# Kernel optimization log

Measured on AMD Instinct MI355X. Metric: run time of the kernel, lower is better.

Reference implementation:

```python
import jax, jax.numpy as jnp
import numpy as np
from jax import lax

EPS = 1e-5

def quantize_ternary(w):
    # scale = mean(|w|).clamp_min(1e-5) computed on detached weight
    scale = jnp.maximum(jnp.mean(jnp.abs(lax.stop_gradient(w))), EPS)
    ws = w / scale
    # STE: forward uses round+clamp, backward is identity in ws
    wq = lax.stop_gradient(jnp.clip(jnp.round(ws), -1.0, 1.0) - ws) + ws
    return wq * scale

def conv2d(x, w, b):
    # x: [N,C,H,W], w: [O,I,kh,kw], stride 1, pad 1 -> same spatial size
    out = lax.conv_general_dilated(
        x, w, window_strides=(1, 1), padding=[(1, 1), (1, 1)],
        dimension_numbers=("NCHW", "OIHW", "NCHW"))
    return out + b[None, :, None, None]

def setup_inputs() -> dict:
    key = jax.random.key(0)
    k1, k2, k3, k4, k5 = jax.random.split(key, 5)
    N, C_in, C_out, H, W, K = 16, 64, 64, 128, 128, 3
    fan_in = C_in * K * K
    bound = 1.0 / np.sqrt(fan_in)
    x = jax.random.normal(k1, (N, C_in, H, W), dtype=jnp.float32)
    w = jax.random.uniform(k2, (C_out, C_in, K, K), minval=-bound, maxval=bound, dtype=jnp.float32)
    b = jax.random.uniform(k3, (C_out,), minval=-bound, maxval=bound, dtype=jnp.float32)
    # growth child: kaiming-uniform-like init scaled by 0.01, zero bias
    w_child = jax.random.uniform(k4, (C_out, C_in, K, K), minval=-bound, maxval=bound, dtype=jnp.float32) * 0.01
    b_child = jnp.zeros((C_out,), dtype=jnp.float32)
    gate = jnp.zeros((1,), dtype=jnp.float32)  # growth_gate buffer
    return {"x": x, "w": w, "b": b, "w_child": w_child, "b_child": b_child, "gate": gate}

def reference(x, w, b, w_child, b_child, gate):
    out = conv2d(x, quantize_ternary(w), b)
    child_out = conv2d(x, quantize_ternary(w_child), b_child)
    g = jax.nn.sigmoid(gate)  # shape [1], broadcasts
    return out + g * child_out
```

## Files before the change

kernel.cpp:

```cpp
#include <hip/hip_runtime.h>
#include <math.h>


typedef __attribute__((ext_vector_type(8))) short short8;
typedef __attribute__((ext_vector_type(4))) float float4v;

__device__ inline unsigned short f2bf(float f) {
  union { float f; unsigned u; } v; v.f = f;
  unsigned u = v.u;
  return (unsigned short)((u + 0x7FFFu + ((u >> 16) & 1u)) >> 16);
}

__global__ __launch_bounds__(256) void prep(
    const float* __restrict__ w, const float* __restrict__ wc,
    const float* __restrict__ b, const float* __restrict__ bc,
    const float* __restrict__ gate,
    unsigned short* __restrict__ wq, float* __restrict__ beff) {
  const int tid = threadIdx.x;
  const float4v* w4 = (const float4v*)w;
  const float4v* c4 = (const float4v*)wc;
  double a0 = 0, a1 = 0, a2 = 0, a3 = 0;
  double c0 = 0, c1 = 0, c2 = 0, c3 = 0;
#pragma unroll
  for (int i = 0; i < 36; i += 4) {
    float4v wa = w4[tid + (i + 0) * 256];
    float4v wb = w4[tid + (i + 1) * 256];
    float4v wcv = w4[tid + (i + 2) * 256];
    float4v wd = w4[tid + (i + 3) * 256];
    float4v xa = c4[tid + (i + 0) * 256];
    float4v xb = c4[tid + (i + 1) * 256];
    float4v xc = c4[tid + (i + 2) * 256];
    float4v xd = c4[tid + (i + 3) * 256];
    a0 += (double)fabsf(wa[0]) + (double)fabsf(wa[1]) + (double)fabsf(wa[2]) + (double)fabsf(wa[3]);
    a1 += (double)fabsf(wb[0]) + (double)fabsf(wb[1]) + (double)fabsf(wb[2]) + (double)fabsf(wb[3]);
    a2 += (double)fabsf(wcv[0]) + (double)fabsf(wcv[1]) + (double)fabsf(wcv[2]) + (double)fabsf(wcv[3]);
    a3 += (double)fabsf(wd[0]) + (double)fabsf(wd[1]) + (double)fabsf(wd[2]) + (double)fabsf(wd[3]);
    c0 += (double)fabsf(xa[0]) + (double)fabsf(xa[1]) + (double)fabsf(xa[2]) + (double)fabsf(xa[3]);
    c1 += (double)fabsf(xb[0]) + (double)fabsf(xb[1]) + (double)fabsf(xb[2]) + (double)fabsf(xb[3]);
    c2 += (double)fabsf(xc[0]) + (double)fabsf(xc[1]) + (double)fabsf(xc[2]) + (double)fabsf(xc[3]);
    c3 += (double)fabsf(xd[0]) + (double)fabsf(xd[1]) + (double)fabsf(xd[2]) + (double)fabsf(xd[3]);
  }
  double a = (a0 + a1) + (a2 + a3);
  double c = (c0 + c1) + (c2 + c3);
#pragma unroll
  for (int off = 32; off > 0; off >>= 1) {
    a += __shfl_down(a, off);
    c += __shfl_down(c, off);
  }
  __shared__ double sa[4], sc[4];
  const int wv = tid >> 6;
  if ((tid & 63) == 0) { sa[wv] = a; sc[wv] = c; }
  __syncthreads();
  const double ta = (sa[0] + sa[1]) + (sa[2] + sa[3]);
  const double tc = (sc[0] + sc[1]) + (sc[2] + sc[3]);
  const float sw = fmaxf((float)(ta * (1.0 / 36864.0)), 1e-5f);
  const float scl = fmaxf((float)(tc * (1.0 / 36864.0)), 1e-5f);
  const float g = 1.0f / (1.0f + expf(-gate[0]));
  const int idx = blockIdx.x * 256 + tid;
  const int tap = idx >> 12;
  const int oc = (idx >> 6) & 63;
  const int ci = idx & 63;
  const int src = oc * 576 + ci * 9 + tap;
  float q1 = fminf(1.f, fmaxf(-1.f, rintf(w[src] / sw))) * sw;
  float q2 = fminf(1.f, fmaxf(-1.f, rintf(wc[src] / scl))) * scl;
  wq[idx] = f2bf(q1 + g * q2);
  if (idx < 64) beff[idx] = b[idx] + g * bc[idx];
}

__global__ __launch_bounds__(512, 4) void conv_fused(
    const float* __restrict__ x, const unsigned short* __restrict__ wq,
    const float* __restrict__ beff, float* __restrict__ out) {
  extern __shared__ __align__(16) char smem[];
  char* Abase = smem;
  char* Bbase = smem + 65536;

  const int bid = blockIdx.x;
  const int xcd = bid & 7;
  const int u = bid >> 3;
  const int n = xcd * 2 + (u >> 6);
  const int h0 = (u & 63) * 2;
  const int tid = threadIdx.x;
  const int lane = tid & 63;
  const int wv = tid >> 6;
  const int rw = wv >> 2;
  const int pxh = ((wv >> 1) & 1) * 64;
  const int och = (wv & 1) * 32;
  const int ln15 = lane & 15;
  const int lq = lane >> 4;

  const float* xn = x + (size_t)n * (64 * 16384);

  const short8 b0v = *(const short8*)(wq + tid * 8);

  const int pxc = tid & 127;
  const int hi = tid >> 7;
#pragma unroll
  for (int grp = 0; grp < 2; ++grp) {
    float t[4][8];
#pragma unroll
    for (int j = 0; j < 4; ++j) {
      const int k = grp * 16 + j * 4 + hi;
      const int r = k >> 3;
      const int c = k & 7;
      const int h = h0 + r - 1;
      if ((unsigned)h < 128u) {
        const float* sp = xn + c * 8 * 16384 + h * 128 + pxc;
#pragma unroll
        for (int e = 0; e < 8; ++e) t[j][e] = sp[e * 16384];
      } else {
#pragma unroll
        for (int e = 0; e < 8; ++e) t[j][e] = 0.f;
      }
    }
#pragma unroll
    for (int j = 0; j < 4; ++j) {
      const int k = grp * 16 + j * 4 + hi;
      const int r = k >> 3;
      const int c = k & 7;
      short8 v;
#pragma unroll
      for (int e = 0; e < 8; ++e) v[e] = (short)f2bf(t[j][e]);
      const int slot = ((r * 128 + pxc) << 3) + (c ^ ((pxc + 1) & 7));
      *(short8*)(Abase + (slot << 4)) = v;
    }
  }

  const int oc0 = tid >> 3;
  const int c0 = tid & 7;
  const int bs0 = (oc0 << 3) + (c0 ^ (oc0 & 7));
  *(short8*)(Bbase + (bs0 << 4)) = b0v;
  __syncthreads();

  float4v acc[4][2] = {};

#pragma unroll
  for (int tap = 0; tap < 9; ++tap) {
    const int dh = tap / 3;
    const int dw = tap - dh * 3;
    const int r = rw + dh;
    const int pb = pxh + ln15 + dw;
    const bool p0 = (pb == 0);
    const bool p129 = (pb == 81);
    const int a0 = (((r * 128 + pb - 1) << 3) + (lq ^ (pb & 7))) << 4;
    const int off0 = p0 ? 2048 : 0;
    const int off3 = p129 ? 4096 : 6144;

    short8 Ab[2][4], Bb[2][2];
#pragma unroll
    for (int cc = 0; cc < 2; ++cc) {
      const int ax = a0 ^ (cc << 6);
      Ab[cc][0] = *(const short8*)(Abase + (ax + off0));
      Ab[cc][1] = *(const short8*)(Abase + (ax + 2048));
      Ab[cc][2] = *(const short8*)(Abase + (ax + 4096));
      Ab[cc][3] = *(const short8*)(Abase + (ax + off3));
      if (p0) Ab[cc][0] = (short8)0;
      if (p129) Ab[cc][3] = (short8)0;
    }
#pragma unroll
    for (int qd = 0; qd < 2; ++qd) {
      const int oc8 = (och + (qd << 4) + ln15) << 3;
      const int k7 = ln15 & 7;
      Bb[0][qd] = *(const short8*)(Bbase + ((oc8 + (lq ^ k7)) << 4));
      Bb[1][qd] = *(const short8*)(Bbase + ((oc8 + ((lq + 4) ^ k7)) << 4));
    }

    if (tap < 8) __syncthreads();

    short8 btv;
    if (tap < 8) btv = *(const short8*)(wq + (tap + 1) * 4096 + tid * 8);

    __builtin_amdgcn_s_setprio(1);
#pragma unroll
    for (int cc2 = 0; cc2 < 2; ++cc2)
#pragma unroll
      for (int mf = 0; mf < 4; ++mf)
#pragma unroll
        for (int qd = 0; qd < 2; ++qd)
          acc[mf][qd] = __builtin_amdgcn_mfma_f32_16x16x32_bf16(
              Ab[cc2][mf], Bb[cc2][qd], acc[mf][qd], 0, 0, 0);
    __builtin_amdgcn_s_setprio(0);

    if (tap < 8) {
      *(short8*)(Bbase + (bs0 << 4)) = btv;
      __syncthreads();
    }
  }

  const int rq = lane >> 4;
  float bias[2];
#pragma unroll
  for (int q = 0; q < 2; ++q) bias[q] = beff[och + q * 16 + ln15];
#pragma unroll
  for (int mf = 0; mf < 4; ++mf) {
#pragma unroll
    for (int qd = 0; qd < 2; ++qd) {
      float4v v = acc[mf][qd] + bias[qd];
      int oc = och + qd * 16 + ln15;
      float* op = out + (((n * 64 + oc) * 128 + h0 + rw) * 128 + pxh + mf * 16 + rq * 4);
      *(float4v*)op = v;
    }
  }
}

extern "C" void kernel_launch(void* const* d_in, const int* in_sizes, int n_in,
                              void* d_out, int out_size, void* d_ws, size_t ws_size,
                              hipStream_t stream) {
  const float* x = (const float*)d_in[0];
  const float* w = (const float*)d_in[1];
  const float* b = (const float*)d_in[2];
  const float* wc = (const float*)d_in[3];
  const float* bc = (const float*)d_in[4];
  const float* gate = (const float*)d_in[5];

  unsigned short* wq = (unsigned short*)d_ws;
  float* beff = (float*)((char*)d_ws + 73728);

  prep<<<144, 256, 0, stream>>>(w, wc, b, bc, gate, wq, beff);
  conv_fused<<<1024, 512, 73728, stream>>>(x, wq, beff, (float*)d_out);
}
```

Baseline: 143.2 us.

## Load weight fragments directly from global into registers, drop LDS staging

Removes the shared-memory staging of per-tap weight tiles and the two barriers per tap. Each lane now loads its B fragments directly from global/L2 with a register double buffer that prefetches the next tap. LDS usage drops from 72KB to 64KB, which may allow more resident blocks. In exchange, weights are read redundantly per wave from cache, and register pressure rises.

```diff
diff --git a/kernel.cpp b/kernel.cpp
--- a/kernel.cpp
+++ b/kernel.cpp
@@ -72,7 +72,6 @@
     const float* __restrict__ beff, float* __restrict__ out) {
   extern __shared__ __align__(16) char smem[];
   char* Abase = smem;
-  char* Bbase = smem + 65536;
 
   const int bid = blockIdx.x;
   const int xcd = bid & 7;
@@ -90,8 +89,6 @@
 
   const float* xn = x + (size_t)n * (64 * 16384);
 
-  const short8 b0v = *(const short8*)(wq + tid * 8);
-
   const int pxc = tid & 127;
   const int hi = tid >> 7;
 #pragma unroll
@@ -124,17 +121,31 @@
       *(short8*)(Abase + (slot << 4)) = v;
     }
   }
-
-  const int oc0 = tid >> 3;
-  const int c0 = tid & 7;
-  const int bs0 = (oc0 << 3) + (c0 ^ (oc0 & 7));
-  *(short8*)(Bbase + (bs0 << 4)) = b0v;
   __syncthreads();
 
+  const unsigned short* wb = wq + (och + ln15) * 64 + lq * 8;
+
   float4v acc[4][2] = {};
+  short8 B[2][2][2];
+
+#pragma unroll
+  for (int qd = 0; qd < 2; ++qd) {
+    B[0][0][qd] = *(const short8*)(wb + qd * 1024);
+    B[0][1][qd] = *(const short8*)(wb + qd * 1024 + 32);
+  }
 
 #pragma unroll
   for (int tap = 0; tap < 9; ++tap) {
+    const int cur = tap & 1, nxt = cur ^ 1;
+    if (tap < 8) {
+      const unsigned short* wn = wb + (tap + 1) * 4096;
+#pragma unroll
+      for (int qd = 0; qd < 2; ++qd) {
+        B[nxt][0][qd] = *(const short8*)(wn + qd * 1024);
+        B[nxt][1][qd] = *(const short8*)(wn + qd * 1024 + 32);
+      }
+    }
+
     const int dh = tap / 3;
     const int dw = tap - dh * 3;
     const int r = rw + dh;
@@ -145,7 +156,7 @@
     const int off0 = p0 ? 2048 : 0;
     const int off3 = p129 ? 4096 : 6144;
 
-    short8 Ab[2][4], Bb[2][2];
+    short8 Ab[2][4];
 #pragma unroll
     for (int cc = 0; cc < 2; ++cc) {
       const int ax = a0 ^ (cc << 6);
@@ -156,18 +167,6 @@
       if (p0) Ab[cc][0] = (short8)0;
       if (p129) Ab[cc][3] = (short8)0;
     }
-#pragma unroll
-    for (int qd = 0; qd < 2; ++qd) {
-      const int oc8 = (och + (qd << 4) + ln15) << 3;
-      const int k7 = ln15 & 7;
-      Bb[0][qd] = *(const short8*)(Bbase + ((oc8 + (lq ^ k7)) << 4));
-      Bb[1][qd] = *(const short8*)(Bbase + ((oc8 + ((lq + 4) ^ k7)) << 4));
-    }
-
-    if (tap < 8) __syncthreads();
-
-    short8 btv;
-    if (tap < 8) btv = *(const short8*)(wq + (tap + 1) * 4096 + tid * 8);
 
     __builtin_amdgcn_s_setprio(1);
 #pragma unroll
@@ -177,13 +176,8 @@
 #pragma unroll
         for (int qd = 0; qd < 2; ++qd)
           acc[mf][qd] = __builtin_amdgcn_mfma_f32_16x16x32_bf16(
-              Ab[cc2][mf], Bb[cc2][qd], acc[mf][qd], 0, 0, 0);
+              Ab[cc2][mf], B[cur][cc2][qd], acc[mf][qd], 0, 0, 0);
     __builtin_amdgcn_s_setprio(0);
-
-    if (tap < 8) {
-      *(short8*)(Bbase + (bs0 << 4)) = btv;
-      __syncthreads();
-    }
   }
 
   const int rq = lane >> 4;
@@ -216,5 +210,5 @@
   float* beff = (float*)((char*)d_ws + 73728);
 
   prep<<<144, 256, 0, stream>>>(w, wc, b, bc, gate, wq, beff);
-  conv_fused<<<1024, 512, 73728, stream>>>(x, wq, beff, (float*)d_out);
-}
+  conv_fused<<<1024, 512, 65536, stream>>>(x, wq, beff, (float*)d_out);
+}
```

New measurement: 159.4 us. 1.11x slower.
